# Kernel tuning notes

Hardware: AMD Instinct MI355X
Metric: run time of the kernel (lower is better)

## Reference

```python
import jax, jax.numpy as jnp
import numpy as np

EPS = 1e-4

def setup_inputs() -> dict:
    key = jax.random.key(0)
    k1, k2, k3 = jax.random.split(key, 3)
    batch, keysize, dict_size, categories = 4096, 512, 16384, 100
    x = jax.random.normal(k1, (batch, keysize), dtype=jnp.float32)
    keys = jax.random.normal(k2, (dict_size, keysize), dtype=jnp.float32) * 0.1  # TruncatedNormal(0, 0.1) approx
    values = jax.random.uniform(k3, (dict_size, categories), dtype=jnp.float32)
    return {"x": x, "keys": keys, "values": values}


def reference(x, keys, values):
    # sq_distance(keys, x): (dict_size, batch)
    kk = jnp.sum(keys * keys, axis=1)[:, None]          # (D, 1)
    xx = jnp.sum(x * x, axis=1)[None, :]                # (1, B)
    d = kk - 2.0 * jnp.matmul(keys, x.T) + xx           # (D, B)
    kern = 1.0 / (d + EPS)                              # reciprocal kernel
    # transpose -> (B, D), matmul values (D, C) -> (B, C)
    return jnp.matmul(kern.T, values)
```

## Files before the change

### kernel.cpp

```cpp
#include <hip/hip_runtime.h>
#include <hip/hip_bf16.h>
#include <cstdint>


#define BSZ   4096
#define DSZ   16384
#define KSZ   512
#define CC    100
#define CP    128
#define EPSV  1e-4f

#define BM     128
#define BD     64
#define DSPLIT 8
#define DCHUNK (DSZ / DSPLIT)
#define NITER  (DCHUNK / BD)
#define KC     256
#define KTS    72

typedef short  short8 __attribute__((ext_vector_type(8)));
typedef float  f32x4  __attribute__((ext_vector_type(4)));
typedef unsigned int   u32;
typedef unsigned short u16;

__device__ __forceinline__ u16 f2bf(float f) {
    union { float f; u32 u; } cv; cv.f = f;
    u32 u = cv.u;
    u += 0x7fffu + ((u >> 16) & 1u);
    return (u16)(u >> 16);
}
__device__ __forceinline__ u32 pack2(float a, float b) {
    return (u32)f2bf(a) | ((u32)f2bf(b) << 16);
}

__device__ __forceinline__ void gload_lds16(const void* g, void* l) {
    __builtin_amdgcn_global_load_lds(
        (const __attribute__((address_space(1))) u32*)g,
        (__attribute__((address_space(3))) u32*)l, 16, 0, 0);
}


__global__ __launch_bounds__(256)
void convert_xk(const float* __restrict__ x, const float* __restrict__ keys,
                u16* __restrict__ xw, u16* __restrict__ kw,
                float* __restrict__ kk, float* __restrict__ xx)
{
    const int tid = threadIdx.x, wid = tid >> 6, lane = tid & 63;
    const int row = blockIdx.x * 4 + wid;
    const float* src; u16* dst; float* nrm; int r;
    if (row < DSZ) { r = row;       src = keys + (size_t)r * KSZ; dst = kw + (size_t)r * KSZ; nrm = kk + r; }
    else           { r = row - DSZ; src = x    + (size_t)r * KSZ; dst = xw + (size_t)r * KSZ; nrm = xx + r; }

    float4 v0 = *reinterpret_cast<const float4*>(src + lane * 8);
    float4 v1 = *reinterpret_cast<const float4*>(src + lane * 8 + 4);
    float s = v0.x*v0.x + v0.y*v0.y + v0.z*v0.z + v0.w*v0.w
            + v1.x*v1.x + v1.y*v1.y + v1.z*v1.z + v1.w*v1.w;

    uint4 w;
    w.x = pack2(v0.x, v0.y); w.y = pack2(v0.z, v0.w);
    w.z = pack2(v1.x, v1.y); w.w = pack2(v1.z, v1.w);
    const int dcol = ((lane >> 3) << 6) + (((lane & 7) ^ (r & 7)) << 3);
    *reinterpret_cast<uint4*>(dst + dcol) = w;

    s += __shfl_xor(s, 1);  s += __shfl_xor(s, 2);  s += __shfl_xor(s, 4);
    s += __shfl_xor(s, 8);  s += __shfl_xor(s, 16); s += __shfl_xor(s, 32);
    if (lane == 0) *nrm = s;
}

__global__ __launch_bounds__(256)
void convert_v(const float* __restrict__ values, u16* __restrict__ vw)
{
    const int gid = blockIdx.x * 256 + threadIdx.x;
    const int c = gid >> 11;
    const int j = gid & 2047;
    const int dp  = ((j >> 3) << 6) + ((j & 7) << 3);
    const int dsg = ((j >> 3) << 6) + (((j & 7) ^ (c & 7)) << 3);
    uint4 w = make_uint4(0, 0, 0, 0);
    if (c < CC) {
        float f[8];
#pragma unroll
        for (int i = 0; i < 8; ++i) f[i] = values[(size_t)(dsg + i) * CC + c];
        w.x = pack2(f[0], f[1]); w.y = pack2(f[2], f[3]);
        w.z = pack2(f[4], f[5]); w.w = pack2(f[6], f[7]);
    }
    *reinterpret_cast<uint4*>(vw + (size_t)c * DSZ + dp) = w;
}

__global__ __launch_bounds__(512, 2)
void varkeys_fast(const u16* __restrict__ xw, const u16* __restrict__ kw,
                  const u16* __restrict__ vw, const float* __restrict__ kkp,
                  const float* __restrict__ xxp, float* __restrict__ out)
{
    __shared__ __align__(16) u16 ksb0[BD * KC];
    __shared__ __align__(16) u16 ksb1[BD * KC];
    __shared__ __align__(16) u16 kT[BM * KTS];
    __shared__ __align__(16) u16 vT[CP * BD];
    __shared__ float xx_s[BM];

    const int tid  = threadIdx.x;
    const int wid  = tid >> 6;
    const int lane = tid & 63;
    const int lo   = lane & 15;
    const int hi   = lane >> 4;
    const int wm   = wid >> 1;
    const int wn   = wid & 1;

    const int h  = blockIdx.x;
    const int by = h & 7, bx = h >> 3;
    const int bm0   = bx * BM;
    const int dbase = by * DCHUNK;

    if (tid < BM) xx_s[tid] = xxp[bm0 + tid];

    short8 xf[2][16];
    {
        const int rbase = bm0 + wm * 32 + lo;
#pragma unroll
        for (int m = 0; m < 2; ++m) {
            const int row = rbase + m * 16;
            const size_t roff = (size_t)row * KSZ;
            const int rs = (row & 7) << 3;
#pragma unroll
            for (int t = 0; t < 16; ++t) {
                const int col = (t * 32 + hi * 8) ^ rs;
                xf[m][t] = *reinterpret_cast<const short8*>(xw + roff + col);
            }
        }
    }

    f32x4 accO[2][4];
#pragma unroll
    for (int m = 0; m < 2; ++m)
#pragma unroll
        for (int n = 0; n < 4; ++n) accO[m][n] = f32x4{0.f, 0.f, 0.f, 0.f};

#pragma unroll
    for (int i = 0; i < 4; ++i) {
        const int ci = wid * 4 + i, flat = ci * 512 + lane * 8;
        gload_lds16(kw + (size_t)(dbase + (flat >> 8)) * KSZ + (flat & 255),
                    (char*)ksb0 + ci * 1024);
    }
    asm volatile("s_waitcnt lgkmcnt(0)" ::: "memory");
    __builtin_amdgcn_s_barrier();

    const int swz = (lo & 7) << 3;

#define PHASE_A(CHUNK, KSBUF)                                                        \
    {                                                                                \
        _Pragma("unroll")                                                            \
        for (int j = 0; j < 8; ++j) {                                                \
            const int k0 = (j * 32 + hi * 8) ^ swz;                                  \
            short8 b0 = *reinterpret_cast<const short8*>(&KSBUF[(wn*32 + lo)*KC + k0]);      \
            short8 b1 = *reinterpret_cast<const short8*>(&KSBUF[(wn*32 + 16 + lo)*KC + k0]); \
            accS[0][0] = __builtin_amdgcn_mfma_f32_16x16x32_bf16(xf[0][(CHUNK)*8+j], b0, accS[0][0], 0,0,0); \
            accS[1][0] = __builtin_amdgcn_mfma_f32_16x16x32_bf16(xf[1][(CHUNK)*8+j], b0, accS[1][0], 0,0,0); \
            accS[0][1] = __builtin_amdgcn_mfma_f32_16x16x32_bf16(xf[0][(CHUNK)*8+j], b1, accS[0][1], 0,0,0); \
            accS[1][1] = __builtin_amdgcn_mfma_f32_16x16x32_bf16(xf[1][(CHUNK)*8+j], b1, accS[1][1], 0,0,0); \
        }                                                                            \
    }

    for (int it = 0; it < NITER; ++it) {
        const int d0 = dbase + it * BD;

        f32x4 accS[2][2];
#pragma unroll
        for (int m = 0; m < 2; ++m)
#pragma unroll
            for (int n = 0; n < 2; ++n) accS[m][n] = f32x4{0.f, 0.f, 0.f, 0.f};

        __builtin_amdgcn_s_barrier();
#pragma unroll
        for (int i = 0; i < 4; ++i) {
            const int ci = wid * 4 + i, flat = ci * 512 + lane * 8;
            gload_lds16(kw + (size_t)(d0 + (flat >> 8)) * KSZ + KC + (flat & 255),
                        (char*)ksb1 + ci * 1024);
        }
#pragma unroll
        for (int i = 0; i < 2; ++i) {
            const int ci = wid * 2 + i, flat = ci * 512 + lane * 8;
            gload_lds16(vw + (size_t)(flat >> 6) * DSZ + d0 + (flat & 63),
                        (char*)vT + ci * 1024);
        }
        const float kkf0 = kkp[d0 + wn * 32 + lo];
        const float kkf1 = kkp[d0 + wn * 32 + 16 + lo];
        asm volatile("s_waitcnt vmcnt(8)" ::: "memory");
        __builtin_amdgcn_s_barrier();
        __builtin_amdgcn_sched_barrier(0);
        PHASE_A(0, ksb0)

        __builtin_amdgcn_s_barrier();
        if (it < NITER - 1) {
            const int nd0 = d0 + BD;
#pragma unroll
            for (int i = 0; i < 4; ++i) {
                const int ci = wid * 4 + i, flat = ci * 512 + lane * 8;
                gload_lds16(kw + (size_t)(nd0 + (flat >> 8)) * KSZ + (flat & 255),
                            (char*)ksb0 + ci * 1024);
            }
            asm volatile("s_waitcnt vmcnt(4)" ::: "memory");
        } else {
            asm volatile("s_waitcnt vmcnt(0)" ::: "memory");
        }
        __builtin_amdgcn_s_barrier();
        __builtin_amdgcn_sched_barrier(0);
        PHASE_A(1, ksb1)

#pragma unroll
        for (int m = 0; m < 2; ++m)
#pragma unroll
            for (int n = 0; n < 2; ++n) {
                const int dl = wn * 32 + n * 16 + lo;
                const float kkv = n ? kkf1 : kkf0;
#pragma unroll
                for (int r = 0; r < 4; ++r) {
                    const int rowl = wm * 32 + m * 16 + hi * 4 + r;
                    const float dsq = kkv + xx_s[rowl] - 2.f * accS[m][n][r] + EPSV;
                    kT[rowl * KTS + dl] = f2bf(__builtin_amdgcn_rcpf(dsq));
                }
            }
        asm volatile("s_waitcnt lgkmcnt(0)" ::: "memory");
        __builtin_amdgcn_s_barrier();
        __builtin_amdgcn_sched_barrier(0);

#pragma unroll
        for (int kst = 0; kst < 2; ++kst) {
            const int k0l = kst * 32 + hi * 8;
            const int k0v = k0l ^ swz;
            short8 a0 = *reinterpret_cast<const short8*>(&kT[(wm * 32 + lo) * KTS + k0l]);
            short8 a1 = *reinterpret_cast<const short8*>(&kT[(wm * 32 + 16 + lo) * KTS + k0l]);
            short8 b[4];
#pragma unroll
            for (int n = 0; n < 4; ++n)
                b[n] = *reinterpret_cast<const short8*>(&vT[(wn * 64 + n * 16 + lo) * BD + k0v]);
#pragma unroll
            for (int n = 0; n < 4; ++n) {
                accO[0][n] = __builtin_amdgcn_mfma_f32_16x16x32_bf16(a0, b[n], accO[0][n], 0, 0, 0);
                accO[1][n] = __builtin_amdgcn_mfma_f32_16x16x32_bf16(a1, b[n], accO[1][n], 0, 0, 0);
            }
        }
    }

#pragma unroll
    for (int m = 0; m < 2; ++m)
#pragma unroll
        for (int n = 0; n < 4; ++n) {
            const int c = wn * 64 + n * 16 + lo;
            if (c < CC) {
#pragma unroll
                for (int r = 0; r < 4; ++r) {
                    const int b_ = bm0 + wm * 32 + m * 16 + hi * 4 + r;
                    atomicAdd(&out[(size_t)b_ * CC + c], accO[m][n][r]);
                }
            }
        }
#undef PHASE_A
}


#define XS_STRIDE 72
#define KS_STRIDE 72
#define KT_STRIDE 72
#define VL_STRIDE 106
#define FKC 64
#define FNKC (KSZ / FKC)

__global__ __launch_bounds__(256)
void varkeys_pre(const float* __restrict__ x, const float* __restrict__ keys,
                 float* __restrict__ kk, float* __restrict__ xx)
{
    const int tid  = threadIdx.x;
    const int wid  = tid >> 6;
    const int lane = tid & 63;
    const int lo   = lane & 15;
    const int sub  = lane >> 4;
    const int row  = blockIdx.x * 16 + wid * 4 + sub;
    const float* src = (row < DSZ) ? keys + (size_t)row * KSZ
                                   : x + (size_t)(row - DSZ) * KSZ;
    float s = 0.f;
#pragma unroll
    for (int j = 0; j < 8; ++j) {
        float4 v = *reinterpret_cast<const float4*>(src + j * 64 + lo * 4);
        s += v.x * v.x + v.y * v.y + v.z * v.z + v.w * v.w;
    }
    s += __shfl_xor(s, 1); s += __shfl_xor(s, 2);
    s += __shfl_xor(s, 4); s += __shfl_xor(s, 8);
    if (lo == 0) {
        if (row < DSZ) kk[row] = s;
        else           xx[row - DSZ] = s;
    }
}

__global__ __launch_bounds__(256, 2)
void varkeys_main(const float* __restrict__ x, const float* __restrict__ keys,
                  const float* __restrict__ values, float* __restrict__ out,
                  const float* __restrict__ kk_ws, const float* __restrict__ xx_ws,
                  int use_ws)
{
    __shared__ __align__(16) u16 xs[BM * XS_STRIDE];
    __shared__ __align__(16) u16 ks[BD * KS_STRIDE];
    __shared__ __align__(16) u16 kTf[BM * KT_STRIDE];
    __shared__ __align__(16) u16 vls[BD * VL_STRIDE];
    __shared__ float kk_s[DCHUNK];
    __shared__ float xx_s[BM];

    const int tid  = threadIdx.x;
    const int wid  = tid >> 6;
    const int lane = tid & 63;
    const int lo   = lane & 15;
    const int hi   = lane >> 4;
    const int wm   = wid >> 1;
    const int wn   = wid & 1;
    const int bm0   = blockIdx.x * BM;
    const int dbase = blockIdx.y * DCHUNK;

    if (use_ws) {
        for (int i = tid; i < DCHUNK; i += 256) kk_s[i] = kk_ws[dbase + i];
        if (tid < BM) xx_s[tid] = xx_ws[bm0 + tid];
    } else {
        for (int rbase = wid * 4; rbase < DCHUNK + BM; rbase += 16) {
            const int row = rbase + hi;
            const float* src = (row < DCHUNK)
                ? keys + (size_t)(dbase + row) * KSZ
                : x + (size_t)(bm0 + row - DCHUNK) * KSZ;
            float s = 0.f;
#pragma unroll
            for (int j = 0; j < 8; ++j) {
                float4 v = *reinterpret_cast<const float4*>(src + j * 64 + lo * 4);
                s += v.x * v.x + v.y * v.y + v.z * v.z + v.w * v.w;
            }
            s += __shfl_xor(s, 1); s += __shfl_xor(s, 2);
            s += __shfl_xor(s, 4); s += __shfl_xor(s, 8);
            if (lo == 0) {
                if (row < DCHUNK) kk_s[row] = s;
                else              xx_s[row - DCHUNK] = s;
            }
        }
    }
    __syncthreads();

    f32x4 accO[4][4];
#pragma unroll
    for (int m = 0; m < 4; ++m)
#pragma unroll
        for (int n = 0; n < 4; ++n) accO[m][n] = f32x4{0.f, 0.f, 0.f, 0.f};

    for (int it = 0; it < NITER; ++it) {
        const int d0 = dbase + it * BD;

        f32x4 accS[4][2];
#pragma unroll
        for (int m = 0; m < 4; ++m)
#pragma unroll
            for (int n = 0; n < 2; ++n) accS[m][n] = f32x4{0.f, 0.f, 0.f, 0.f};

        for (int kc = 0; kc < FNKC; ++kc) {
            __syncthreads();
#pragma unroll
            for (int j = 0; j < 8; ++j) {
                const int idx = tid + j * 256;
                const int row = idx >> 4, c4 = idx & 15;
                float4 v = *reinterpret_cast<const float4*>(
                    x + (size_t)(bm0 + row) * KSZ + kc * FKC + c4 * 4);
                u32* dst = reinterpret_cast<u32*>(&xs[row * XS_STRIDE + c4 * 4]);
                dst[0] = pack2(v.x, v.y); dst[1] = pack2(v.z, v.w);
            }
#pragma unroll
            for (int j = 0; j < 4; ++j) {
                const int idx = tid + j * 256;
                const int row = idx >> 4, c4 = idx & 15;
                float4 v = *reinterpret_cast<const float4*>(
                    keys + (size_t)(d0 + row) * KSZ + kc * FKC + c4 * 4);
                u32* dst = reinterpret_cast<u32*>(&ks[row * KS_STRIDE + c4 * 4]);
                dst[0] = pack2(v.x, v.y); dst[1] = pack2(v.z, v.w);
            }
            __syncthreads();
#pragma unroll
            for (int kst = 0; kst < 2; ++kst) {
                const int k0 = kst * 32 + hi * 8;
                short8 a[4], b[2];
#pragma unroll
                for (int m = 0; m < 4; ++m)
                    a[m] = *reinterpret_cast<const short8*>(
                        &xs[(wm * 64 + m * 16 + lo) * XS_STRIDE + k0]);
#pragma unroll
                for (int n = 0; n < 2; ++n)
                    b[n] = *reinterpret_cast<const short8*>(
                        &ks[(wn * 32 + n * 16 + lo) * KS_STRIDE + k0]);
#pragma unroll
                for (int m = 0; m < 4; ++m)
#pragma unroll
                    for (int n = 0; n < 2; ++n)
                        accS[m][n] = __builtin_amdgcn_mfma_f32_16x16x32_bf16(
                            a[m], b[n], accS[m][n], 0, 0, 0);
            }
        }

#pragma unroll
        for (int m = 0; m < 4; ++m)
#pragma unroll
            for (int n = 0; n < 2; ++n) {
                const int dl = wn * 32 + n * 16 + lo;
                const float kkv = kk_s[it * BD + dl];
#pragma unroll
                for (int r = 0; r < 4; ++r) {
                    const int bl = wm * 64 + m * 16 + hi * 4 + r;
                    const float dsq = kkv + xx_s[bl] - 2.f * accS[m][n][r] + EPSV;
                    kTf[bl * KT_STRIDE + dl] = f2bf(__builtin_amdgcn_rcpf(dsq));
                }
            }

#pragma unroll
        for (int j = 0; j < 7; ++j) {
            const int idx = tid + j * 256;
            if (idx < 1600) {
                const int row = idx / 25, c4 = idx % 25;
                float4 v = *reinterpret_cast<const float4*>(
                    values + (size_t)(d0 + row) * CC + c4 * 4);
                u32* dst = reinterpret_cast<u32*>(&vls[row * VL_STRIDE + c4 * 4]);
                dst[0] = pack2(v.x, v.y); dst[1] = pack2(v.z, v.w);
            }
        }
        __syncthreads();

#pragma unroll
        for (int ks2 = 0; ks2 < 2; ++ks2) {
            const int k0 = ks2 * 32 + hi * 8;
            short8 a[4], b[4];
#pragma unroll
            for (int m = 0; m < 4; ++m)
                a[m] = *reinterpret_cast<const short8*>(
                    &kTf[(wm * 64 + m * 16 + lo) * KT_STRIDE + k0]);
#pragma unroll
            for (int n = 0; n < 4; ++n) {
                const int c = wn * 64 + n * 16 + lo;
                short8 t = {0, 0, 0, 0, 0, 0, 0, 0};
                if (c < CC) {
#pragma unroll
                    for (int i = 0; i < 8; ++i)
                        t[i] = (short)vls[(k0 + i) * VL_STRIDE + c];
                }
                b[n] = t;
            }
#pragma unroll
            for (int m = 0; m < 4; ++m)
#pragma unroll
                for (int n = 0; n < 4; ++n)
                    accO[m][n] = __builtin_amdgcn_mfma_f32_16x16x32_bf16(
                        a[m], b[n], accO[m][n], 0, 0, 0);
        }
    }

#pragma unroll
    for (int m = 0; m < 4; ++m)
#pragma unroll
        for (int n = 0; n < 4; ++n) {
            const int c = wn * 64 + n * 16 + lo;
            if (c < CC) {
#pragma unroll
                for (int r = 0; r < 4; ++r) {
                    const int b_ = bm0 + wm * 64 + m * 16 + hi * 4 + r;
                    atomicAdd(&out[(size_t)b_ * CC + c], accO[m][n][r]);
                }
            }
        }
}

extern "C" void kernel_launch(void* const* d_in, const int* in_sizes, int n_in,
                              void* d_out, int out_size, void* d_ws, size_t ws_size,
                              hipStream_t stream) {
    const float* x      = (const float*)d_in[0];
    const float* keys   = (const float*)d_in[1];
    const float* values = (const float*)d_in[2];
    float* out = (float*)d_out;

    hipMemsetAsync(d_out, 0, (size_t)out_size * sizeof(float), stream);

    const size_t off_xw = 0;
    const size_t off_kw = off_xw + (size_t)BSZ * KSZ * 2;
    const size_t off_vw = off_kw + (size_t)DSZ * KSZ * 2;
    const size_t off_kk = off_vw + (size_t)CP * DSZ * 2;
    const size_t off_xx = off_kk + (size_t)DSZ * 4;
    const size_t need   = off_xx + (size_t)BSZ * 4;

    if (ws_size >= need) {
        u16* xw = (u16*)((char*)d_ws + off_xw);
        u16* kw = (u16*)((char*)d_ws + off_kw);
        u16* vw = (u16*)((char*)d_ws + off_vw);
        float* kk = (float*)((char*)d_ws + off_kk);
        float* xx = (float*)((char*)d_ws + off_xx);
        convert_xk<<<dim3((DSZ + BSZ) / 4), dim3(256), 0, stream>>>(x, keys, xw, kw, kk, xx);
        convert_v<<<dim3((CP * DSZ / 8) / 256), dim3(256), 0, stream>>>(values, vw);
        varkeys_fast<<<dim3(DSPLIT * (BSZ / BM)), dim3(512), 0, stream>>>(xw, kw, vw, kk, xx, out);
    } else {
        const size_t ws_need = (size_t)(DSZ + BSZ) * sizeof(float);
        const int use_ws = (ws_size >= ws_need) ? 1 : 0;
        float* kk = (float*)d_ws;
        float* xx = kk + DSZ;
        if (use_ws) {
            varkeys_pre<<<dim3((DSZ + BSZ) / 16), dim3(256), 0, stream>>>(x, keys, kk, xx);
        }
        varkeys_main<<<dim3(BSZ / BM, DSPLIT), dim3(256), 0, stream>>>(
            x, keys, values, out, kk, xx, use_ws);
    }
}
```

Baseline: 134.9 us.

## Switch distance GEMM to FP8 MFMA and double D-split with higher occupancy

Result: slower. 193.0 us (+43.1%).

```diff
diff --git a/kernel.cpp b/kernel.cpp
--- a/kernel.cpp
+++ b/kernel.cpp
@@ -1,5 +1,6 @@
 #include <hip/hip_runtime.h>
 #include <hip/hip_bf16.h>
+#include <hip/hip_fp8.h>
 #include <cstdint>
 
 
@@ -12,16 +13,17 @@
 
 #define BM     128
 #define BD     64
-#define DSPLIT 8
+#define DSPLIT 16
 #define DCHUNK (DSZ / DSPLIT)
 #define NITER  (DCHUNK / BD)
-#define KC     256
 #define KTS    72
 
 typedef short  short8 __attribute__((ext_vector_type(8)));
 typedef float  f32x4  __attribute__((ext_vector_type(4)));
+typedef long   lng2   __attribute__((ext_vector_type(2)));
 typedef unsigned int   u32;
 typedef unsigned short u16;
+typedef unsigned char  u8;
 
 __device__ __forceinline__ u16 f2bf(float f) {
     union { float f; u32 u; } cv; cv.f = f;
@@ -32,6 +34,10 @@
 __device__ __forceinline__ u32 pack2(float a, float b) {
     return (u32)f2bf(a) | ((u32)f2bf(b) << 16);
 }
+__device__ __forceinline__ u8 f2fp8(float f) {
+    __hip_fp8_e4m3 t(f);
+    return *reinterpret_cast<u8*>(&t);
+}
 
 __device__ __forceinline__ void gload_lds16(const void* g, void* l) {
     __builtin_amdgcn_global_load_lds(
@@ -42,12 +48,12 @@
 
 __global__ __launch_bounds__(256)
 void convert_xk(const float* __restrict__ x, const float* __restrict__ keys,
-                u16* __restrict__ xw, u16* __restrict__ kw,
+                u8* __restrict__ xw, u8* __restrict__ kw,
                 float* __restrict__ kk, float* __restrict__ xx)
 {
     const int tid = threadIdx.x, wid = tid >> 6, lane = tid & 63;
     const int row = blockIdx.x * 4 + wid;
-    const float* src; u16* dst; float* nrm; int r;
+    const float* src; u8* dst; float* nrm; int r;
     if (row < DSZ) { r = row;       src = keys + (size_t)r * KSZ; dst = kw + (size_t)r * KSZ; nrm = kk + r; }
     else           { r = row - DSZ; src = x    + (size_t)r * KSZ; dst = xw + (size_t)r * KSZ; nrm = xx + r; }
 
@@ -56,11 +62,20 @@
     float s = v0.x*v0.x + v0.y*v0.y + v0.z*v0.z + v0.w*v0.w
             + v1.x*v1.x + v1.y*v1.y + v1.z*v1.z + v1.w*v1.w;
 
-    uint4 w;
-    w.x = pack2(v0.x, v0.y); w.y = pack2(v0.z, v0.w);
-    w.z = pack2(v1.x, v1.y); w.w = pack2(v1.z, v1.w);
-    const int dcol = ((lane >> 3) << 6) + (((lane & 7) ^ (r & 7)) << 3);
-    *reinterpret_cast<uint4*>(dst + dcol) = w;
+    unsigned long long pk = 0;
+    pk |= (unsigned long long)f2fp8(v0.x);
+    pk |= (unsigned long long)f2fp8(v0.y) << 8;
+    pk |= (unsigned long long)f2fp8(v0.z) << 16;
+    pk |= (unsigned long long)f2fp8(v0.w) << 24;
+    pk |= (unsigned long long)f2fp8(v1.x) << 32;
+    pk |= (unsigned long long)f2fp8(v1.y) << 40;
+    pk |= (unsigned long long)f2fp8(v1.z) << 48;
+    pk |= (unsigned long long)f2fp8(v1.w) << 56;
+
+    const int j = lane >> 2, hi_l = lane & 3;
+    const int ch = j >> 3, jl = j & 7, jj = jl >> 1, f = jl & 1;
+    const int off = ch * 256 + (((jj * 64 + hi_l * 16)) ^ ((r & 7) << 4)) + f * 8;
+    *reinterpret_cast<unsigned long long*>(dst + off) = pk;
 
     s += __shfl_xor(s, 1);  s += __shfl_xor(s, 2);  s += __shfl_xor(s, 4);
     s += __shfl_xor(s, 8);  s += __shfl_xor(s, 16); s += __shfl_xor(s, 32);
@@ -86,13 +101,13 @@
     *reinterpret_cast<uint4*>(vw + (size_t)c * DSZ + dp) = w;
 }
 
-__global__ __launch_bounds__(512, 2)
-void varkeys_fast(const u16* __restrict__ xw, const u16* __restrict__ kw,
+__global__ __launch_bounds__(512, 4)
+void varkeys_fast(const u8* __restrict__ xw, const u8* __restrict__ kw,
                   const u16* __restrict__ vw, const float* __restrict__ kkp,
                   const float* __restrict__ xxp, float* __restrict__ out)
 {
-    __shared__ __align__(16) u16 ksb0[BD * KC];
-    __shared__ __align__(16) u16 ksb1[BD * KC];
+    __shared__ __align__(16) u8  ksb0[BD * 256];
+    __shared__ __align__(16) u8  ksb1[BD * 256];
     __shared__ __align__(16) u16 kT[BM * KTS];
     __shared__ __align__(16) u16 vT[CP * BD];
     __shared__ float xx_s[BM];
@@ -106,25 +121,26 @@
     const int wn   = wid & 1;
 
     const int h  = blockIdx.x;
-    const int by = h & 7, bx = h >> 3;
+    const int by = (h & 7) * 2 + ((h >> 3) & 1);
+    const int bx = h >> 4;
     const int bm0   = bx * BM;
     const int dbase = by * DCHUNK;
 
     if (tid < BM) xx_s[tid] = xxp[bm0 + tid];
 
-    short8 xf[2][16];
+    lng2 xq[2][8];
     {
-        const int rbase = bm0 + wm * 32 + lo;
 #pragma unroll
         for (int m = 0; m < 2; ++m) {
-            const int row = rbase + m * 16;
-            const size_t roff = (size_t)row * KSZ;
-            const int rs = (row & 7) << 3;
-#pragma unroll
-            for (int t = 0; t < 16; ++t) {
-                const int col = (t * 32 + hi * 8) ^ rs;
-                xf[m][t] = *reinterpret_cast<const short8*>(xw + roff + col);
-            }
+            const int row = bm0 + wm * 32 + m * 16 + lo;
+            const u8* base = xw + (size_t)row * KSZ;
+            const int s16 = (row & 7) << 4;
+#pragma unroll
+            for (int ch = 0; ch < 2; ++ch)
+#pragma unroll
+                for (int jj = 0; jj < 4; ++jj)
+                    xq[m][ch * 4 + jj] = *reinterpret_cast<const lng2*>(
+                        base + ch * 256 + ((jj * 64 + hi * 16) ^ s16));
         }
     }
 
@@ -134,29 +150,50 @@
 #pragma unroll
         for (int n = 0; n < 4; ++n) accO[m][n] = f32x4{0.f, 0.f, 0.f, 0.f};
 
-#pragma unroll
-    for (int i = 0; i < 4; ++i) {
-        const int ci = wid * 4 + i, flat = ci * 512 + lane * 8;
-        gload_lds16(kw + (size_t)(dbase + (flat >> 8)) * KSZ + (flat & 255),
-                    (char*)ksb0 + ci * 1024);
-    }
+#define IS_KS(BUFP, DK, CCH) { \
+        _Pragma("unroll") \
+        for (int i = 0; i < 2; ++i) { \
+            const int ci = wid * 2 + i; \
+            const int flat = ci * 1024 + lane * 16; \
+            gload_lds16(kw + (size_t)((DK) + (flat >> 8)) * KSZ + (CCH) * 256 + (flat & 255), \
+                        (char*)(BUFP) + ci * 1024); \
+        } }
+
+#define IS_VT(D0) { \
+        _Pragma("unroll") \
+        for (int i = 0; i < 2; ++i) { \
+            const int ci = wid * 2 + i; \
+            const int flat = ci * 512 + lane * 8; \
+            gload_lds16(vw + (size_t)(flat >> 6) * DSZ + (D0) + (flat & 63), \
+                        (char*)vT + ci * 1024); \
+        } }
+
+    IS_KS(ksb0, dbase, 0)
     asm volatile("s_waitcnt lgkmcnt(0)" ::: "memory");
     __builtin_amdgcn_s_barrier();
 
-    const int swz = (lo & 7) << 3;
-
-#define PHASE_A(CHUNK, KSBUF)                                                        \
-    {                                                                                \
-        _Pragma("unroll")                                                            \
-        for (int j = 0; j < 8; ++j) {                                                \
-            const int k0 = (j * 32 + hi * 8) ^ swz;                                  \
-            short8 b0 = *reinterpret_cast<const short8*>(&KSBUF[(wn*32 + lo)*KC + k0]);      \
-            short8 b1 = *reinterpret_cast<const short8*>(&KSBUF[(wn*32 + 16 + lo)*KC + k0]); \
-            accS[0][0] = __builtin_amdgcn_mfma_f32_16x16x32_bf16(xf[0][(CHUNK)*8+j], b0, accS[0][0], 0,0,0); \
-            accS[1][0] = __builtin_amdgcn_mfma_f32_16x16x32_bf16(xf[1][(CHUNK)*8+j], b0, accS[1][0], 0,0,0); \
-            accS[0][1] = __builtin_amdgcn_mfma_f32_16x16x32_bf16(xf[0][(CHUNK)*8+j], b1, accS[0][1], 0,0,0); \
-            accS[1][1] = __builtin_amdgcn_mfma_f32_16x16x32_bf16(xf[1][(CHUNK)*8+j], b1, accS[1][1], 0,0,0); \
-        }                                                                            \
+    const int swz   = (lo & 7) << 3;
+    const int swz16 = (lo & 7) << 4;
+
+#define A16(CH, BUF)                                                                  \
+    {                                                                                 \
+        _Pragma("unroll")                                                             \
+        for (int jj = 0; jj < 4; ++jj) {                                              \
+            const int off = (jj * 64 + hi * 16) ^ swz16;                              \
+            const u8* p0 = (const u8*)(BUF) + (wn * 32 + lo) * 256 + off;             \
+            lng2 b0 = *reinterpret_cast<const lng2*>(p0);                             \
+            lng2 b1 = *reinterpret_cast<const lng2*>(p0 + 16 * 256);                  \
+            lng2 a0 = xq[0][(CH) * 4 + jj];                                           \
+            lng2 a1 = xq[1][(CH) * 4 + jj];                                           \
+            accS[0][0] = __builtin_amdgcn_mfma_f32_16x16x32_fp8_fp8(a0[0], b0[0], accS[0][0], 0, 0, 0); \
+            accS[1][0] = __builtin_amdgcn_mfma_f32_16x16x32_fp8_fp8(a1[0], b0[0], accS[1][0], 0, 0, 0); \
+            accS[0][1] = __builtin_amdgcn_mfma_f32_16x16x32_fp8_fp8(a0[0], b1[0], accS[0][1], 0, 0, 0); \
+            accS[1][1] = __builtin_amdgcn_mfma_f32_16x16x32_fp8_fp8(a1[0], b1[0], accS[1][1], 0, 0, 0); \
+            accS[0][0] = __builtin_amdgcn_mfma_f32_16x16x32_fp8_fp8(a0[1], b0[1], accS[0][0], 0, 0, 0); \
+            accS[1][0] = __builtin_amdgcn_mfma_f32_16x16x32_fp8_fp8(a1[1], b0[1], accS[1][0], 0, 0, 0); \
+            accS[0][1] = __builtin_amdgcn_mfma_f32_16x16x32_fp8_fp8(a0[1], b1[1], accS[0][1], 0, 0, 0); \
+            accS[1][1] = __builtin_amdgcn_mfma_f32_16x16x32_fp8_fp8(a1[1], b1[1], accS[1][1], 0, 0, 0); \
+        }                                                                             \
     }
 
     for (int it = 0; it < NITER; ++it) {
@@ -169,41 +206,25 @@
             for (int n = 0; n < 2; ++n) accS[m][n] = f32x4{0.f, 0.f, 0.f, 0.f};
 
         __builtin_amdgcn_s_barrier();
-#pragma unroll
-        for (int i = 0; i < 4; ++i) {
-            const int ci = wid * 4 + i, flat = ci * 512 + lane * 8;
-            gload_lds16(kw + (size_t)(d0 + (flat >> 8)) * KSZ + KC + (flat & 255),
-                        (char*)ksb1 + ci * 1024);
-        }
-#pragma unroll
-        for (int i = 0; i < 2; ++i) {
-            const int ci = wid * 2 + i, flat = ci * 512 + lane * 8;
-            gload_lds16(vw + (size_t)(flat >> 6) * DSZ + d0 + (flat & 63),
-                        (char*)vT + ci * 1024);
-        }
+        IS_KS(ksb1, d0, 1)
+        IS_VT(d0)
         const float kkf0 = kkp[d0 + wn * 32 + lo];
         const float kkf1 = kkp[d0 + wn * 32 + 16 + lo];
-        asm volatile("s_waitcnt vmcnt(8)" ::: "memory");
+        asm volatile("s_waitcnt vmcnt(6)" ::: "memory");
         __builtin_amdgcn_s_barrier();
         __builtin_amdgcn_sched_barrier(0);
-        PHASE_A(0, ksb0)
+        A16(0, ksb0)
 
         __builtin_amdgcn_s_barrier();
         if (it < NITER - 1) {
-            const int nd0 = d0 + BD;
-#pragma unroll
-            for (int i = 0; i < 4; ++i) {
-                const int ci = wid * 4 + i, flat = ci * 512 + lane * 8;
-                gload_lds16(kw + (size_t)(nd0 + (flat >> 8)) * KSZ + (flat & 255),
-                            (char*)ksb0 + ci * 1024);
-            }
-            asm volatile("s_waitcnt vmcnt(4)" ::: "memory");
+            IS_KS(ksb0, d0 + BD, 0)
+            asm volatile("s_waitcnt vmcnt(6)" ::: "memory");
         } else {
             asm volatile("s_waitcnt vmcnt(0)" ::: "memory");
         }
         __builtin_amdgcn_s_barrier();
         __builtin_amdgcn_sched_barrier(0);
-        PHASE_A(1, ksb1)
+        A16(1, ksb1)
 
 #pragma unroll
         for (int m = 0; m < 2; ++m)
@@ -218,6 +239,7 @@
                     kT[rowl * KTS + dl] = f2bf(__builtin_amdgcn_rcpf(dsq));
                 }
             }
+        asm volatile("s_waitcnt vmcnt(2)" ::: "memory");
         asm volatile("s_waitcnt lgkmcnt(0)" ::: "memory");
         __builtin_amdgcn_s_barrier();
         __builtin_amdgcn_sched_barrier(0);
@@ -228,14 +250,14 @@
             const int k0v = k0l ^ swz;
             short8 a0 = *reinterpret_cast<const short8*>(&kT[(wm * 32 + lo) * KTS + k0l]);
             short8 a1 = *reinterpret_cast<const short8*>(&kT[(wm * 32 + 16 + lo) * KTS + k0l]);
-            short8 b[4];
-#pragma unroll
-            for (int n = 0; n < 4; ++n)
-                b[n] = *reinterpret_cast<const short8*>(&vT[(wn * 64 + n * 16 + lo) * BD + k0v]);
-#pragma unroll
-            for (int n = 0; n < 4; ++n) {
-                accO[0][n] = __builtin_amdgcn_mfma_f32_16x16x32_bf16(a0, b[n], accO[0][n], 0, 0, 0);
-                accO[1][n] = __builtin_amdgcn_mfma_f32_16x16x32_bf16(a1, b[n], accO[1][n], 0, 0, 0);
+#pragma unroll
+            for (int nh = 0; nh < 2; ++nh) {
+                short8 b0 = *reinterpret_cast<const short8*>(&vT[(wn * 64 + nh * 32 + lo) * BD + k0v]);
+                short8 b1 = *reinterpret_cast<const short8*>(&vT[(wn * 64 + nh * 32 + 16 + lo) * BD + k0v]);
+                accO[0][nh * 2 + 0] = __builtin_amdgcn_mfma_f32_16x16x32_bf16(a0, b0, accO[0][nh * 2 + 0], 0, 0, 0);
+                accO[1][nh * 2 + 0] = __builtin_amdgcn_mfma_f32_16x16x32_bf16(a1, b0, accO[1][nh * 2 + 0], 0, 0, 0);
+                accO[0][nh * 2 + 1] = __builtin_amdgcn_mfma_f32_16x16x32_bf16(a0, b1, accO[0][nh * 2 + 1], 0, 0, 0);
+                accO[1][nh * 2 + 1] = __builtin_amdgcn_mfma_f32_16x16x32_bf16(a1, b1, accO[1][nh * 2 + 1], 0, 0, 0);
             }
         }
     }
@@ -253,7 +275,9 @@
                 }
             }
         }
-#undef PHASE_A
+#undef IS_KS
+#undef IS_VT
+#undef A16
 }
 
 
@@ -263,6 +287,9 @@
 #define VL_STRIDE 106
 #define FKC 64
 #define FNKC (KSZ / FKC)
+#define FDSPLIT 8
+#define FDCHUNK (DSZ / FDSPLIT)
+#define FNITER  (FDCHUNK / BD)
 
 __global__ __launch_bounds__(256)
 void varkeys_pre(const float* __restrict__ x, const float* __restrict__ keys,
@@ -300,7 +327,7 @@
     __shared__ __align__(16) u16 ks[BD * KS_STRIDE];
     __shared__ __align__(16) u16 kTf[BM * KT_STRIDE];
     __shared__ __align__(16) u16 vls[BD * VL_STRIDE];
-    __shared__ float kk_s[DCHUNK];
+    __shared__ float kk_s[FDCHUNK];
     __shared__ float xx_s[BM];
 
     const int tid  = threadIdx.x;
@@ -311,17 +338,17 @@
     const int wm   = wid >> 1;
     const int wn   = wid & 1;
     const int bm0   = blockIdx.x * BM;
-    const int dbase = blockIdx.y * DCHUNK;
+    const int dbase = blockIdx.y * FDCHUNK;
 
     if (use_ws) {
-        for (int i = tid; i < DCHUNK; i += 256) kk_s[i] = kk_ws[dbase + i];
+        for (int i = tid; i < FDCHUNK; i += 256) kk_s[i] = kk_ws[dbase + i];
         if (tid < BM) xx_s[tid] = xx_ws[bm0 + tid];
     } else {
-        for (int rbase = wid * 4; rbase < DCHUNK + BM; rbase += 16) {
+        for (int rbase = wid * 4; rbase < FDCHUNK + BM; rbase += 16) {
             const int row = rbase + hi;
-            const float* src = (row < DCHUNK)
+            const float* src = (row < FDCHUNK)
                 ? keys + (size_t)(dbase + row) * KSZ
-                : x + (size_t)(bm0 + row - DCHUNK) * KSZ;
+                : x + (size_t)(bm0 + row - FDCHUNK) * KSZ;
             float s = 0.f;
 #pragma unroll
             for (int j = 0; j < 8; ++j) {
@@ -331,8 +358,8 @@
             s += __shfl_xor(s, 1); s += __shfl_xor(s, 2);
             s += __shfl_xor(s, 4); s += __shfl_xor(s, 8);
             if (lo == 0) {
-                if (row < DCHUNK) kk_s[row] = s;
-                else              xx_s[row - DCHUNK] = s;
+                if (row < FDCHUNK) kk_s[row] = s;
+                else               xx_s[row - FDCHUNK] = s;
             }
         }
     }
@@ -344,7 +371,7 @@
 #pragma unroll
         for (int n = 0; n < 4; ++n) accO[m][n] = f32x4{0.f, 0.f, 0.f, 0.f};
 
-    for (int it = 0; it < NITER; ++it) {
+    for (int it = 0; it < FNITER; ++it) {
         const int d0 = dbase + it * BD;
 
         f32x4 accS[4][2];
@@ -476,15 +503,15 @@
     hipMemsetAsync(d_out, 0, (size_t)out_size * sizeof(float), stream);
 
     const size_t off_xw = 0;
-    const size_t off_kw = off_xw + (size_t)BSZ * KSZ * 2;
-    const size_t off_vw = off_kw + (size_t)DSZ * KSZ * 2;
+    const size_t off_kw = off_xw + (size_t)BSZ * KSZ;
+    const size_t off_vw = off_kw + (size_t)DSZ * KSZ;
     const size_t off_kk = off_vw + (size_t)CP * DSZ * 2;
     const size_t off_xx = off_kk + (size_t)DSZ * 4;
     const size_t need   = off_xx + (size_t)BSZ * 4;
 
     if (ws_size >= need) {
-        u16* xw = (u16*)((char*)d_ws + off_xw);
-        u16* kw = (u16*)((char*)d_ws + off_kw);
+        u8*  xw = (u8*)((char*)d_ws + off_xw);
+        u8*  kw = (u8*)((char*)d_ws + off_kw);
         u16* vw = (u16*)((char*)d_ws + off_vw);
         float* kk = (float*)((char*)d_ws + off_kk);
         float* xx = (float*)((char*)d_ws + off_xx);
@@ -499,7 +526,7 @@
         if (use_ws) {
             varkeys_pre<<<dim3((DSZ + BSZ) / 16), dim3(256), 0, stream>>>(x, keys, kk, xx);
         }
-        varkeys_main<<<dim3(BSZ / BM, DSPLIT), dim3(256), 0, stream>>>(
+        varkeys_main<<<dim3(BSZ / BM, FDSPLIT), dim3(256), 0, stream>>>(
             x, keys, values, out, kk, xx, use_ws);
     }
 }
```
